# Kernel optimization log

Hardware: AMD Instinct MI355X
Metric: run time of the kernel (lower is better)

## Reference

```python
import jax, jax.numpy as jnp
import numpy as np

N_GENES = 20000
N_CELLS = 1024   # expression_dim
FM_DIM = 512     # scgpt_embed_dim
EMB = 512        # embed_dim == projection_dim
N_EDGES = 640000
EPS = 1e-5


def _layernorm(x, g, b):
    mu = jnp.mean(x, axis=-1, keepdims=True)
    var = jnp.mean((x - mu) ** 2, axis=-1, keepdims=True)
    return (x - mu) * jax.lax.rsqrt(var + EPS) * g + b


def _sage_conv(x, src, dst, Wl, bl, Wr):
    # PyG SAGEConv (mean aggr): lin_l(mean_{j in N(i)} x_j) + lin_r(x_i)
    n = x.shape[0]
    agg = jax.ops.segment_sum(x[src], dst, num_segments=n)          # [N, F]
    cnt = jax.ops.segment_sum(jnp.ones((src.shape[0],), x.dtype), dst, num_segments=n)
    mean = agg / jnp.maximum(cnt, 1.0)[:, None]
    return mean @ Wl.T + bl + x @ Wr.T


def setup_inputs() -> dict:
    key = jax.random.key(0)
    ks = jax.random.split(key, 20)
    s = 0.02
    inp = {
        'x_foundation': jax.random.normal(ks[0], (N_GENES, FM_DIM), jnp.float32),
        'x_expression': jax.random.normal(ks[1], (N_GENES, N_CELLS), jnp.float32),
        'ppi_edge_index': jax.random.randint(ks[2], (2, N_EDGES), 0, N_GENES, jnp.int32),
        # expression SAGE layer 0 (N_CELLS -> EMB)
        'Wl0': s * jax.random.normal(ks[3], (EMB, N_CELLS), jnp.float32),
        'bl0': jnp.zeros((EMB,), jnp.float32),
        'Wr0': s * jax.random.normal(ks[4], (EMB, N_CELLS), jnp.float32),
        # expression SAGE layer 1 (EMB -> EMB)
        'Wl1': s * jax.random.normal(ks[5], (EMB, EMB), jnp.float32),
        'bl1': jnp.zeros((EMB,), jnp.float32),
        'Wr1': s * jax.random.normal(ks[6], (EMB, EMB), jnp.float32),
        # foundation projection: Linear + LayerNorm
        'Wf': s * jax.random.normal(ks[7], (EMB, FM_DIM), jnp.float32),
        'bf': jnp.zeros((EMB,), jnp.float32),
        'g1': jnp.ones((EMB,), jnp.float32),
        'b1': jnp.zeros((EMB,), jnp.float32),
        # fusion layer: Linear + LayerNorm
        'Wfu': s * jax.random.normal(ks[8], (EMB, EMB), jnp.float32),
        'bfu': jnp.zeros((EMB,), jnp.float32),
        'g2': jnp.ones((EMB,), jnp.float32),
        'b2': jnp.zeros((EMB,), jnp.float32),
        # final SAGE layer (EMB -> EMB), max(1, num_layers//2) == 1 layer
        'Wl2': s * jax.random.normal(ks[9], (EMB, EMB), jnp.float32),
        'bl2': jnp.zeros((EMB,), jnp.float32),
        'Wr2': s * jax.random.normal(ks[10], (EMB, EMB), jnp.float32),
    }
    return inp


def reference(x_foundation, x_expression, ppi_edge_index,
              Wl0, bl0, Wr0, Wl1, bl1, Wr1,
              Wf, bf, g1, b1, Wfu, bfu, g2, b2,
              Wl2, bl2, Wr2):
    src, dst = ppi_edge_index[0], ppi_edge_index[1]
    # expression branch: SAGEConv -> ELU (dropout = identity in eval)
    h = jax.nn.elu(_sage_conv(x_expression, src, dst, Wl0, bl0, Wr0))
    h = jax.nn.elu(_sage_conv(h, src, dst, Wl1, bl1, Wr1))
    # foundation branch: Linear -> LayerNorm -> GELU (exact, as torch nn.GELU)
    f = jax.nn.gelu(_layernorm(x_foundation @ Wf.T + bf, g1, b1), approximate=False)
    # add fusion, then Linear -> LayerNorm -> SiLU
    fused = h + f
    fo = jax.nn.silu(_layernorm(fused @ Wfu.T + bfu, g2, b2))
    # final SAGE layer(s): SAGEConv -> ELU
    gene_emb = jax.nn.elu(_sage_conv(fo, src, dst, Wl2, bl2, Wr2))
    return gene_emb
```

## Files before the change

### kernel.cpp

```cpp
#include <hip/hip_runtime.h>
#include <hip/hip_bf16.h>
#include <math.h>

#define N_GENES 20000
#define N_CELLS 1024
#define FM_DIM  512
#define EMB     512
#define N_EDGES 640000
#define LN_EPS  1e-5f
#define SCAN_B  79
#define IDX_CAP 2560

typedef __attribute__((ext_vector_type(8))) short bf8;
typedef __attribute__((ext_vector_type(4))) float f32x4;

__device__ __forceinline__ float bflo(unsigned v) { return __uint_as_float(v << 16); }
__device__ __forceinline__ float bfhi(unsigned v) { return __uint_as_float(v & 0xffff0000u); }
__device__ __forceinline__ unsigned short f2bf(float f) {
    unsigned u = __float_as_uint(f);
    return (unsigned short)((u + 0x7fffu + ((u >> 16) & 1u)) >> 16);
}
__device__ __forceinline__ unsigned packbf(float x, float y) {
    return (unsigned)f2bf(x) | ((unsigned)f2bf(y) << 16);
}
__device__ __forceinline__ unsigned addbf2(unsigned x, unsigned y) {
    return packbf(bflo(x) + bflo(y), bfhi(x) + bfhi(y));
}
__device__ __forceinline__ uint4 pack8(float4 a, float4 b) {
    uint4 o;
    o.x = packbf(a.x, a.y);
    o.y = packbf(a.z, a.w);
    o.z = packbf(b.x, b.y);
    o.w = packbf(b.z, b.w);
    return o;
}

__device__ __forceinline__ void gload16(const unsigned short* g, unsigned short* l) {
    __builtin_amdgcn_global_load_lds(
        (const __attribute__((address_space(1))) unsigned int*)g,
        (__attribute__((address_space(3))) unsigned int*)l, 16, 0, 0);
}

__global__ __launch_bounds__(256) void k_cvtcnt(const float4* __restrict__ xe,
                                                const float4* s0, const float4* s1,
                                                const float4* s2, const float4* s3,
                                                const float4* s4, const float4* s5,
                                                const float4* s6, const float4* s7,
                                                uint4* __restrict__ Xe,
                                                uint4* __restrict__ Wb,
                                                const int* __restrict__ edst,
                                                int* __restrict__ cnt,
                                                unsigned char* __restrict__ eslot) {
    if (blockIdx.x < 2048) {
        for (int i = blockIdx.x * 256 + threadIdx.x; i < 2560000 + 327680;
             i += 2048 * 256) {
            if (i < 2560000) {
                Xe[i] = pack8(xe[2 * i], xe[2 * i + 1]);
            } else {
                int w = i - 2560000;
                const float4* src; int off;
                if (w < 65536)       { src = s0; off = w; }
                else if (w < 131072) { src = s1; off = w - 65536; }
                else if (w < 163840) { src = s2; off = w - 131072; }
                else if (w < 196608) { src = s3; off = w - 163840; }
                else if (w < 229376) { src = s4; off = w - 196608; }
                else if (w < 262144) { src = s5; off = w - 229376; }
                else if (w < 294912) { src = s6; off = w - 262144; }
                else                 { src = s7; off = w - 294912; }
                Wb[w] = pack8(src[2 * off], src[2 * off + 1]);
            }
        }
    } else {
        int e = (blockIdx.x - 2048) * 256 + threadIdx.x;
        if (e < N_EDGES) {
            int old = atomicAdd(&cnt[edst[e]], 1);
            eslot[e] = (unsigned char)old;
        }
    }
}

__global__ __launch_bounds__(256) void k_scan1(const int* __restrict__ cnt,
                                               int* __restrict__ row_ptr,
                                               int* __restrict__ bsum) {
    __shared__ int wsum[4];
    int b = blockIdx.x, t = threadIdx.x;
    int i = b * 256 + t;
    int v = (i < N_GENES) ? cnt[i] : 0;
    int lane = t & 63, wv = t >> 6;
    int x = v;
#pragma unroll
    for (int off = 1; off < 64; off <<= 1) {
        int y = __shfl_up(x, off);
        if (lane >= off) x += y;
    }
    if (lane == 63) wsum[wv] = x;
    __syncthreads();
    if (t == 0) {
        int s = 0;
        for (int w = 0; w < 4; ++w) { int tmp = wsum[w]; wsum[w] = s; s += tmp; }
    }
    __syncthreads();
    int excl = x - v + wsum[wv];
    if (i < N_GENES) row_ptr[i] = excl;
    if (t == 255) bsum[b] = excl + v;
}

__global__ void k_scan2(const int* __restrict__ bsum, int* __restrict__ boff) {
    __shared__ int wsum[2];
    int t = threadIdx.x;
    int v = (t < SCAN_B) ? bsum[t] : 0;
    int lane = t & 63, wv = t >> 6;
    int x = v;
#pragma unroll
    for (int off = 1; off < 64; off <<= 1) {
        int y = __shfl_up(x, off);
        if (lane >= off) x += y;
    }
    if (lane == 63) wsum[wv] = x;
    __syncthreads();
    int add = (wv == 1) ? wsum[0] : 0;
    int excl = x - v + add;
    if (t < SCAN_B) boff[t] = excl;
    if (t == SCAN_B) boff[SCAN_B] = excl;
}

__global__ __launch_bounds__(256) void k_scan3(int* __restrict__ row_ptr,
                                               const int* __restrict__ boff) {
    int i = blockIdx.x * 256 + threadIdx.x;
    if (i < N_GENES) row_ptr[i] += boff[i >> 8];
    if (blockIdx.x == 0 && threadIdx.x == 0) row_ptr[N_GENES] = boff[SCAN_B];
}

__global__ __launch_bounds__(256) void k_gemm_pf(const unsigned short* __restrict__ A,
                                                 const unsigned short* __restrict__ Wl,
                                                 const unsigned short* __restrict__ Wr,
                                                 unsigned short* __restrict__ C0,
                                                 unsigned short* __restrict__ C1,
                                                 int M, int K,
                                                 const int* __restrict__ e_src,
                                                 const int* __restrict__ e_dst,
                                                 const int* __restrict__ row_ptr,
                                                 const unsigned char* __restrict__ eslot,
                                                 int* __restrict__ csr) {
    __shared__ __attribute__((aligned(16))) unsigned short As[3][128][32];
    __shared__ __attribute__((aligned(16))) unsigned short Bs[3][128][32];
    if (blockIdx.y >= 160) {
        int e = ((blockIdx.y - 160) * 8 + blockIdx.x) * 256 + threadIdx.x;
        if (e < N_EDGES) {
            int d = e_dst[e];
            csr[row_ptr[d] + (int)eslot[e]] = e_src[e];
        }
        return;
    }
    int m0 = (blockIdx.x * 20 + (blockIdx.y >> 3)) * 128;
    if (m0 >= M) return;
    int sel = blockIdx.y & 7;
    const unsigned short* W = (sel < 4) ? Wl : Wr;
    unsigned short* Cp = (sel < 4) ? C0 : C1;
    int n0 = (sel & 3) * 128;
    int tid = threadIdx.x;
    int lane = tid & 63;
    int w = tid >> 6, wr = w >> 1, wc = w & 1;

    int srow = tid >> 2, sch = tid & 3;
    int rA0 = min(m0 + srow, M - 1);
    int rA1 = min(m0 + srow + 64, M - 1);
    const unsigned short* gA0 = A + (size_t)rA0 * K + sch * 8;
    const unsigned short* gA1 = A + (size_t)rA1 * K + sch * 8;
    const unsigned short* gB0 = W + (size_t)(n0 + srow) * K + sch * 8;
    const unsigned short* gB1 = W + (size_t)(n0 + srow + 64) * K + sch * 8;

    f32x4 acc[4][4];
#pragma unroll
    for (int i = 0; i < 4; ++i)
#pragma unroll
        for (int j = 0; j < 4; ++j) acc[i][j] = (f32x4){0.f, 0.f, 0.f, 0.f};

    auto stage = [&](int b, int k0) {
        unsigned short* Ab = &As[b][0][0];
        unsigned short* Bb = &Bs[b][0][0];
        gload16(gA0 + k0, Ab + tid * 8);
        gload16(gA1 + k0, Ab + 64 * 32 + tid * 8);
        gload16(gB0 + k0, Bb + tid * 8);
        gload16(gB1 + k0, Bb + 64 * 32 + tid * 8);
    };
    auto compute = [&](int b) {
        const unsigned short* Ab = &As[b][0][0];
        const unsigned short* Bb = &Bs[b][0][0];
        bf8 af[4], bff[4];
#pragma unroll
        for (int f = 0; f < 4; ++f) {
            af[f]  = *(const bf8*)(Ab + (wr * 64 + f * 16 + (lane & 15)) * 32 + (lane >> 4) * 8);
            bff[f] = *(const bf8*)(Bb + (wc * 64 + f * 16 + (lane & 15)) * 32 + (lane >> 4) * 8);
        }
#pragma unroll
        for (int i = 0; i < 4; ++i)
#pragma unroll
            for (int j = 0; j < 4; ++j)
                acc[i][j] = __builtin_amdgcn_mfma_f32_16x16x32_bf16(af[i], bff[j],
                                                                    acc[i][j], 0, 0, 0);
    };

#define PF_STEP(CB, SB, ST, VM)                                  \
    stage(SB, (ST) * 32);                                        \
    asm volatile("s_waitcnt vmcnt(" #VM ")" ::: "memory");       \
    __builtin_amdgcn_s_barrier();                                \
    __builtin_amdgcn_sched_barrier(0);                           \
    compute(CB);                                                 \
    asm volatile("s_waitcnt lgkmcnt(0)" ::: "memory");           \
    __builtin_amdgcn_s_barrier();                                \
    __builtin_amdgcn_sched_barrier(0);

    const int NT = K / 32;
    stage(0, 0);
    stage(1, 32);
    for (int t = 0; t + 4 < NT; t += 3) {
        PF_STEP(0, 2, t + 2, 8)
        PF_STEP(1, 0, t + 3, 8)
        PF_STEP(2, 1, t + 4, 8)
    }
    asm volatile("s_waitcnt vmcnt(4)" ::: "memory");
    __builtin_amdgcn_s_barrier();
    __builtin_amdgcn_sched_barrier(0);
    compute(0);
    asm volatile("s_waitcnt lgkmcnt(0)" ::: "memory");
    __builtin_amdgcn_s_barrier();
    __builtin_amdgcn_sched_barrier(0);
    asm volatile("s_waitcnt vmcnt(0)" ::: "memory");
    __builtin_amdgcn_s_barrier();
    __builtin_amdgcn_sched_barrier(0);
    compute(1);
#undef PF_STEP

#pragma unroll
    for (int i = 0; i < 4; ++i) {
        int rb = m0 + wr * 64 + i * 16 + (lane >> 4) * 4;
#pragma unroll
        for (int j = 0; j < 4; ++j) {
            int cc = n0 + wc * 64 + j * 16 + (lane & 15);
#pragma unroll
            for (int e = 0; e < 4; ++e) {
                int r = rb + e;
                if (r < M) Cp[(size_t)r * EMB + cc] = f2bf(acc[i][j][e]);
            }
        }
    }
}

__global__ __launch_bounds__(256) void k_gemm_fu(const unsigned short* __restrict__ A,
                                                 const unsigned short* __restrict__ A2,
                                                 const unsigned short* __restrict__ W,
                                                 unsigned short* __restrict__ Cp,
                                                 int M, int K) {
    __shared__ __attribute__((aligned(16))) unsigned short As[2][128][32];
    __shared__ __attribute__((aligned(16))) unsigned short Bs[2][128][32];
    int m0 = (blockIdx.x * 20 + (blockIdx.y >> 2)) * 128;
    if (m0 >= M) return;
    int n0 = (blockIdx.y & 3) * 128;
    int tid = threadIdx.x;
    int lane = tid & 63;
    int w = tid >> 6, wr = w >> 1, wc = w & 1;

    int srow = tid >> 2, sch = tid & 3;
    int rA0 = min(m0 + srow, M - 1);
    int rA1 = min(m0 + srow + 64, M - 1);
    const unsigned short* gA0 = A + (size_t)rA0 * K + sch * 8;
    const unsigned short* gA1 = A + (size_t)rA1 * K + sch * 8;
    const unsigned short* hA0 = A2 + (size_t)rA0 * K + sch * 8;
    const unsigned short* hA1 = A2 + (size_t)rA1 * K + sch * 8;
    const unsigned short* gB0 = W + (size_t)(n0 + srow) * K + sch * 8;
    const unsigned short* gB1 = W + (size_t)(n0 + srow + 64) * K + sch * 8;

    f32x4 acc[4][4];
#pragma unroll
    for (int i = 0; i < 4; ++i)
#pragma unroll
        for (int j = 0; j < 4; ++j) acc[i][j] = (f32x4){0.f, 0.f, 0.f, 0.f};

    auto compute = [&](int b) {
        const unsigned short* Ab = &As[b][0][0];
        const unsigned short* Bb = &Bs[b][0][0];
        bf8 af[4], bff[4];
#pragma unroll
        for (int f = 0; f < 4; ++f) {
            af[f]  = *(const bf8*)(Ab + (wr * 64 + f * 16 + (lane & 15)) * 32 + (lane >> 4) * 8);
            bff[f] = *(const bf8*)(Bb + (wc * 64 + f * 16 + (lane & 15)) * 32 + (lane >> 4) * 8);
        }
#pragma unroll
        for (int i = 0; i < 4; ++i)
#pragma unroll
            for (int j = 0; j < 4; ++j)
                acc[i][j] = __builtin_amdgcn_mfma_f32_16x16x32_bf16(af[i], bff[j],
                                                                    acc[i][j], 0, 0, 0);
    };

    for (int k0 = 0; k0 < K; k0 += 64) {
        uint4 x00 = *(const uint4*)(gA0 + k0);
        uint4 y00 = *(const uint4*)(hA0 + k0);
        uint4 x10 = *(const uint4*)(gA1 + k0);
        uint4 y10 = *(const uint4*)(hA1 + k0);
        uint4 x01 = *(const uint4*)(gA0 + k0 + 32);
        uint4 y01 = *(const uint4*)(hA0 + k0 + 32);
        uint4 x11 = *(const uint4*)(gA1 + k0 + 32);
        uint4 y11 = *(const uint4*)(hA1 + k0 + 32);
        uint4 a00, a10, a01, a11;
        a00.x = addbf2(x00.x, y00.x); a00.y = addbf2(x00.y, y00.y);
        a00.z = addbf2(x00.z, y00.z); a00.w = addbf2(x00.w, y00.w);
        a10.x = addbf2(x10.x, y10.x); a10.y = addbf2(x10.y, y10.y);
        a10.z = addbf2(x10.z, y10.z); a10.w = addbf2(x10.w, y10.w);
        a01.x = addbf2(x01.x, y01.x); a01.y = addbf2(x01.y, y01.y);
        a01.z = addbf2(x01.z, y01.z); a01.w = addbf2(x01.w, y01.w);
        a11.x = addbf2(x11.x, y11.x); a11.y = addbf2(x11.y, y11.y);
        a11.z = addbf2(x11.z, y11.z); a11.w = addbf2(x11.w, y11.w);
        __syncthreads();
        *(uint4*)(&As[0][0][0] + tid * 8)       = a00;
        *(uint4*)(&As[0][64][0] + tid * 8)      = a10;
        *(uint4*)(&As[1][0][0] + tid * 8)       = a01;
        *(uint4*)(&As[1][64][0] + tid * 8)      = a11;
        gload16(gB0 + k0,      &Bs[0][0][0] + tid * 8);
        gload16(gB1 + k0,      &Bs[0][64][0] + tid * 8);
        gload16(gB0 + k0 + 32, &Bs[1][0][0] + tid * 8);
        gload16(gB1 + k0 + 32, &Bs[1][64][0] + tid * 8);
        __syncthreads();
        compute(0);
        compute(1);
    }

#pragma unroll
    for (int i = 0; i < 4; ++i) {
        int rb = m0 + wr * 64 + i * 16 + (lane >> 4) * 4;
#pragma unroll
        for (int j = 0; j < 4; ++j) {
            int cc = n0 + wc * 64 + j * 16 + (lane & 15);
#pragma unroll
            for (int e = 0; e < 4; ++e) {
                int r = rb + e;
                if (r < M) Cp[(size_t)r * EMB + cc] = f2bf(acc[i][j][e]);
            }
        }
    }
}

__global__ __launch_bounds__(256) void k_gemm_p(const unsigned short* __restrict__ A,
                                                const unsigned short* __restrict__ Wl,
                                                const unsigned short* __restrict__ Wr,
                                                unsigned short* __restrict__ C0,
                                                unsigned short* __restrict__ C1,
                                                int M, int K) {
    __shared__ __attribute__((aligned(16))) unsigned short As[2][128][32];
    __shared__ __attribute__((aligned(16))) unsigned short Bs[2][128][32];
    int m0 = (blockIdx.x * 20 + (blockIdx.y >> 3)) * 128;
    if (m0 >= M) return;
    int sel = blockIdx.y & 7;
    const unsigned short* W = (sel < 4) ? Wl : Wr;
    unsigned short* Cp = (sel < 4) ? C0 : C1;
    int n0 = (sel & 3) * 128;
    int tid = threadIdx.x;
    int lane = tid & 63;
    int w = tid >> 6, wr = w >> 1, wc = w & 1;

    int srow = tid >> 2, sch = tid & 3;
    int rA0 = min(m0 + srow, M - 1);
    int rA1 = min(m0 + srow + 64, M - 1);
    const unsigned short* gA0 = A + (size_t)rA0 * K + sch * 8;
    const unsigned short* gA1 = A + (size_t)rA1 * K + sch * 8;
    const unsigned short* gB0 = W + (size_t)(n0 + srow) * K + sch * 8;
    const unsigned short* gB1 = W + (size_t)(n0 + srow + 64) * K + sch * 8;

    f32x4 acc[4][4];
#pragma unroll
    for (int i = 0; i < 4; ++i)
#pragma unroll
        for (int j = 0; j < 4; ++j) acc[i][j] = (f32x4){0.f, 0.f, 0.f, 0.f};

    auto compute = [&](int b) {
        const unsigned short* Ab = &As[b][0][0];
        const unsigned short* Bb = &Bs[b][0][0];
        bf8 af[4], bff[4];
#pragma unroll
        for (int f = 0; f < 4; ++f) {
            af[f]  = *(const bf8*)(Ab + (wr * 64 + f * 16 + (lane & 15)) * 32 + (lane >> 4) * 8);
            bff[f] = *(const bf8*)(Bb + (wc * 64 + f * 16 + (lane & 15)) * 32 + (lane >> 4) * 8);
        }
#pragma unroll
        for (int i = 0; i < 4; ++i)
#pragma unroll
            for (int j = 0; j < 4; ++j)
                acc[i][j] = __builtin_amdgcn_mfma_f32_16x16x32_bf16(af[i], bff[j],
                                                                    acc[i][j], 0, 0, 0);
    };

    for (int k0 = 0; k0 < K; k0 += 64) {
        __syncthreads();
        gload16(gA0 + k0,      &As[0][0][0] + tid * 8);
        gload16(gA1 + k0,      &As[0][64][0] + tid * 8);
        gload16(gA0 + k0 + 32, &As[1][0][0] + tid * 8);
        gload16(gA1 + k0 + 32, &As[1][64][0] + tid * 8);
        gload16(gB0 + k0,      &Bs[0][0][0] + tid * 8);
        gload16(gB1 + k0,      &Bs[0][64][0] + tid * 8);
        gload16(gB0 + k0 + 32, &Bs[1][0][0] + tid * 8);
        gload16(gB1 + k0 + 32, &Bs[1][64][0] + tid * 8);
        __syncthreads();
        compute(0);
        compute(1);
    }

#pragma unroll
    for (int i = 0; i < 4; ++i) {
        int rb = m0 + wr * 64 + i * 16 + (lane >> 4) * 4;
#pragma unroll
        for (int j = 0; j < 4; ++j) {
            int cc = n0 + wc * 64 + j * 16 + (lane & 15);
#pragma unroll
            for (int e = 0; e < 4; ++e) {
                int r = rb + e;
                if (r < M) Cp[(size_t)r * EMB + cc] = f2bf(acc[i][j][e]);
            }
        }
    }
}

__global__ __launch_bounds__(256) void k_gemm_3(const unsigned short* __restrict__ A1,
                                                const float* __restrict__ A2,
                                                const unsigned short* __restrict__ Wl,
                                                const unsigned short* __restrict__ Wr,
                                                const unsigned short* __restrict__ Wf,
                                                unsigned short* __restrict__ C0,
                                                unsigned short* __restrict__ C1,
                                                unsigned short* __restrict__ CF,
                                                int M) {
    const int K = 512;
    __shared__ __attribute__((aligned(16))) unsigned short As[2][128][32];
    __shared__ __attribute__((aligned(16))) unsigned short Bs[2][128][32];
    int y = blockIdx.y;
    bool fpath = (y >= 160);
    int m0, n0;
    const unsigned short* W;
    unsigned short* Cp;
    if (!fpath) {
        m0 = (blockIdx.x * 20 + (y >> 3)) * 128;
        int sel = y & 7;
        W = (sel < 4) ? Wl : Wr;
        Cp = (sel < 4) ? C0 : C1;
        n0 = (sel & 3) * 128;
    } else {
        int y2 = y - 160;
        m0 = (blockIdx.x * 20 + (y2 >> 2)) * 128;
        n0 = (y2 & 3) * 128;
        W = Wf;
        Cp = CF;
    }
    if (m0 >= M) return;
    int tid = threadIdx.x;
    int lane = tid & 63;
    int w = tid >> 6, wr = w >> 1, wc = w & 1;

    int srow = tid >> 2, sch = tid & 3;
    int rA0 = min(m0 + srow, M - 1);
    int rA1 = min(m0 + srow + 64, M - 1);
    const unsigned short* gA0 = A1 + (size_t)rA0 * K + sch * 8;
    const unsigned short* gA1 = A1 + (size_t)rA1 * K + sch * 8;
    const float* fA0 = A2 + (size_t)rA0 * K + sch * 8;
    const float* fA1 = A2 + (size_t)rA1 * K + sch * 8;
    const unsigned short* gB0 = W + (size_t)(n0 + srow) * K + sch * 8;
    const unsigned short* gB1 = W + (size_t)(n0 + srow + 64) * K + sch * 8;

    f32x4 acc[4][4];
#pragma unroll
    for (int i = 0; i < 4; ++i)
#pragma unroll
        for (int j = 0; j < 4; ++j) acc[i][j] = (f32x4){0.f, 0.f, 0.f, 0.f};

    auto compute = [&](int b) {
        const unsigned short* Ab = &As[b][0][0];
        const unsigned short* Bb = &Bs[b][0][0];
        bf8 af[4], bff[4];
#pragma unroll
        for (int f = 0; f < 4; ++f) {
            af[f]  = *(const bf8*)(Ab + (wr * 64 + f * 16 + (lane & 15)) * 32 + (lane >> 4) * 8);
            bff[f] = *(const bf8*)(Bb + (wc * 64 + f * 16 + (lane & 15)) * 32 + (lane >> 4) * 8);
        }
#pragma unroll
        for (int i = 0; i < 4; ++i)
#pragma unroll
            for (int j = 0; j < 4; ++j)
                acc[i][j] = __builtin_amdgcn_mfma_f32_16x16x32_bf16(af[i], bff[j],
                                                                    acc[i][j], 0, 0, 0);
    };

    for (int k0 = 0; k0 < K; k0 += 64) {
        float4 f0a, f0b, f0c, f0d, f1a, f1b, f1c, f1d;
        if (fpath) {
            f0a = *(const float4*)(fA0 + k0);      f0b = *(const float4*)(fA0 + k0 + 4);
            f1a = *(const float4*)(fA1 + k0);      f1b = *(const float4*)(fA1 + k0 + 4);
            f0c = *(const float4*)(fA0 + k0 + 32); f0d = *(const float4*)(fA0 + k0 + 36);
            f1c = *(const float4*)(fA1 + k0 + 32); f1d = *(const float4*)(fA1 + k0 + 36);
        }
        __syncthreads();
        if (fpath) {
            *(uint4*)(&As[0][0][0] + tid * 8)  = pack8(f0a, f0b);
            *(uint4*)(&As[0][64][0] + tid * 8) = pack8(f1a, f1b);
            *(uint4*)(&As[1][0][0] + tid * 8)  = pack8(f0c, f0d);
            *(uint4*)(&As[1][64][0] + tid * 8) = pack8(f1c, f1d);
        } else {
            gload16(gA0 + k0,      &As[0][0][0] + tid * 8);
            gload16(gA1 + k0,      &As[0][64][0] + tid * 8);
            gload16(gA0 + k0 + 32, &As[1][0][0] + tid * 8);
            gload16(gA1 + k0 + 32, &As[1][64][0] + tid * 8);
        }
        gload16(gB0 + k0,      &Bs[0][0][0] + tid * 8);
        gload16(gB1 + k0,      &Bs[0][64][0] + tid * 8);
        gload16(gB0 + k0 + 32, &Bs[1][0][0] + tid * 8);
        gload16(gB1 + k0 + 32, &Bs[1][64][0] + tid * 8);
        __syncthreads();
        compute(0);
        compute(1);
    }

#pragma unroll
    for (int i = 0; i < 4; ++i) {
        int rb = m0 + wr * 64 + i * 16 + (lane >> 4) * 4;
#pragma unroll
        for (int j = 0; j < 4; ++j) {
            int cc = n0 + wc * 64 + j * 16 + (lane & 15);
#pragma unroll
            for (int e = 0; e < 4; ++e) {
                int r = rb + e;
                if (r < M) Cp[(size_t)r * EMB + cc] = f2bf(acc[i][j][e]);
            }
        }
    }
}

template <int OUTF32>
__device__ __forceinline__ void sage_body(const unsigned short* yl,
                                          const unsigned short* yr,
                                          const float* bl,
                                          const int* row_ptr,
                                          const int* csr,
                                          void* outp, int slice, int nblk,
                                          int* sIdx) {
    int g = threadIdx.x >> 3;
    int l = threadIdx.x & 7;
    int node = nblk * 32 + g;
    int w = slice * 8 + l;
    int s32 = row_ptr[nblk * 32];
    int e32 = row_ptr[nblk * 32 + 32];
    int nIdx = e32 - s32;
    bool lds_ok = (nIdx <= IDX_CAP);
    if (lds_ok) {
        for (int i = threadIdx.x; i < nIdx; i += 256) sIdx[i] = csr[s32 + i];
    }
    __syncthreads();
    int s = row_ptr[node], e = row_ptr[node + 1];
    int deg = e - s;
    const char* Yb = (const char*)yl;
    unsigned lb = (unsigned)(w << 4);
    float ac[8];
#pragma unroll
    for (int q = 0; q < 8; ++q) ac[q] = 0.f;
    if (lds_ok) {
        int lp = s - s32;
        int p = 0;
        for (; p + 8 <= deg; p += 8) {
            int j[8];
#pragma unroll
            for (int q = 0; q < 8; ++q) j[q] = sIdx[lp + p + q];
            uint4 v[8];
#pragma unroll
            for (int q = 0; q < 8; ++q)
                v[q] = *(const uint4*)(Yb + (((unsigned)j[q] << 10) + lb));
#pragma unroll
            for (int q = 0; q < 8; ++q) {
                ac[0] += bflo(v[q].x); ac[1] += bfhi(v[q].x);
                ac[2] += bflo(v[q].y); ac[3] += bfhi(v[q].y);
                ac[4] += bflo(v[q].z); ac[5] += bfhi(v[q].z);
                ac[6] += bflo(v[q].w); ac[7] += bfhi(v[q].w);
            }
        }
        for (; p < deg; ++p) {
            int j = sIdx[lp + p];
            uint4 v = *(const uint4*)(Yb + (((unsigned)j << 10) + lb));
            ac[0] += bflo(v.x); ac[1] += bfhi(v.x);
            ac[2] += bflo(v.y); ac[3] += bfhi(v.y);
            ac[4] += bflo(v.z); ac[5] += bfhi(v.z);
            ac[6] += bflo(v.w); ac[7] += bfhi(v.w);
        }
    } else {
        for (int p = s; p < e; ++p) {
            int j = csr[p];
            uint4 v = *(const uint4*)(Yb + (((unsigned)j << 10) + lb));
            ac[0] += bflo(v.x); ac[1] += bfhi(v.x);
            ac[2] += bflo(v.y); ac[3] += bfhi(v.y);
            ac[4] += bflo(v.z); ac[5] += bfhi(v.z);
            ac[6] += bflo(v.w); ac[7] += bfhi(v.w);
        }
    }
    float inv = 1.f / fmaxf((float)deg, 1.f);
    uint4 vr = ((const uint4*)yr)[(size_t)node * 64 + w];
    float4 bA = ((const float4*)bl)[2 * w];
    float4 bB = ((const float4*)bl)[2 * w + 1];
    float o[8];
    o[0] = ac[0] * inv + bA.x + bflo(vr.x);
    o[1] = ac[1] * inv + bA.y + bfhi(vr.x);
    o[2] = ac[2] * inv + bA.z + bflo(vr.y);
    o[3] = ac[3] * inv + bA.w + bfhi(vr.y);
    o[4] = ac[4] * inv + bB.x + bflo(vr.z);
    o[5] = ac[5] * inv + bB.y + bfhi(vr.z);
    o[6] = ac[6] * inv + bB.z + bflo(vr.w);
    o[7] = ac[7] * inv + bB.w + bfhi(vr.w);
#pragma unroll
    for (int q = 0; q < 8; ++q) o[q] = o[q] > 0.f ? o[q] : expm1f(o[q]);
    if (OUTF32) {
        float4* O = (float4*)outp;
        O[(size_t)node * 128 + 2 * w]     = make_float4(o[0], o[1], o[2], o[3]);
        O[(size_t)node * 128 + 2 * w + 1] = make_float4(o[4], o[5], o[6], o[7]);
    } else {
        uint4 ov;
        ov.x = packbf(o[0], o[1]);
        ov.y = packbf(o[2], o[3]);
        ov.z = packbf(o[4], o[5]);
        ov.w = packbf(o[6], o[7]);
        ((uint4*)outp)[(size_t)node * 64 + w] = ov;
    }
}

template <int OUTF32>
__global__ __launch_bounds__(256) void k_sage_b(const unsigned short* __restrict__ yl,
                                                const unsigned short* __restrict__ yr,
                                                const float* __restrict__ bl,
                                                const int* __restrict__ row_ptr,
                                                const int* __restrict__ csr,
                                                void* __restrict__ outp) {
    __shared__ int sIdx[IDX_CAP];
    sage_body<OUTF32>(yl, yr, bl, row_ptr, csr, outp, blockIdx.x, blockIdx.y, sIdx);
}

template <int ACT>
__device__ __forceinline__ void ln_body(const unsigned short* X,
                                        const float* bias, const float* g,
                                        const float* b, unsigned short* Y, int row) {
    __shared__ float red[8];
    int t = threadIdx.x;
    unsigned v = *(const unsigned*)(X + (size_t)row * EMB + 2 * t);
    float x0 = bflo(v) + bias[2 * t];
    float x1 = bfhi(v) + bias[2 * t + 1];
    float s = x0 + x1;
    float q = x0 * x0 + x1 * x1;
#pragma unroll
    for (int off = 32; off > 0; off >>= 1) {
        s += __shfl_down(s, off);
        q += __shfl_down(q, off);
    }
    int wave = t >> 6, lane = t & 63;
    if (lane == 0) { red[wave * 2] = s; red[wave * 2 + 1] = q; }
    __syncthreads();
    if (t == 0) {
        float ts = 0.f, tq = 0.f;
        for (int w = 0; w < 4; w++) { ts += red[w * 2]; tq += red[w * 2 + 1]; }
        red[0] = ts; red[1] = tq;
    }
    __syncthreads();
    float mu   = red[0] * (1.0f / 512.0f);
    float var  = red[1] * (1.0f / 512.0f) - mu * mu;
    float rstd = rsqrtf(var + LN_EPS);
    float y0 = (x0 - mu) * rstd * g[2 * t]     + b[2 * t];
    float y1 = (x1 - mu) * rstd * g[2 * t + 1] + b[2 * t + 1];
    if (ACT == 0) {
        y0 = 0.5f * y0 * (1.0f + erff(y0 * 0.70710678118654752440f));
        y1 = 0.5f * y1 * (1.0f + erff(y1 * 0.70710678118654752440f));
    } else {
        y0 = y0 / (1.0f + expf(-y0));
        y1 = y1 / (1.0f + expf(-y1));
    }
    ((unsigned*)Y)[(size_t)row * (EMB / 2) + t] = packbf(y0, y1);
}

template <int ACT>
__global__ __launch_bounds__(256) void k_ln_b(const unsigned short* __restrict__ X,
                                              const float* __restrict__ bias,
                                              const float* __restrict__ g,
                                              const float* __restrict__ b,
                                              unsigned short* __restrict__ Y) {
    ln_body<ACT>(X, bias, g, b, Y, blockIdx.x);
}

__global__ __launch_bounds__(256) void k_sageln(const unsigned short* __restrict__ C0,
                                                const unsigned short* __restrict__ C1,
                                                const float* __restrict__ bl1,
                                                const int* __restrict__ row_ptr,
                                                const int* __restrict__ csr,
                                                unsigned short* __restrict__ Pd,
                                                const unsigned short* __restrict__ F0,
                                                const float* __restrict__ bf_,
                                                const float* __restrict__ g1,
                                                const float* __restrict__ b1,
                                                unsigned short* __restrict__ fout) {
    __shared__ int sIdx[IDX_CAP];
    if (blockIdx.y < 625) {
        sage_body<0>(C0, C1, bl1, row_ptr, csr, Pd, blockIdx.x, blockIdx.y, sIdx);
    } else {
        ln_body<0>(F0, bf_, g1, b1, fout, (blockIdx.y - 625) * 8 + blockIdx.x);
    }
}

extern "C" void kernel_launch(void* const* d_in, const int* in_sizes, int n_in,
                              void* d_out, int out_size, void* d_ws, size_t ws_size,
                              hipStream_t stream) {
    const float* x_found = (const float*)d_in[0];
    const float* x_exp   = (const float*)d_in[1];
    const int*   ppi     = (const int*)d_in[2];
    const float* Wl0 = (const float*)d_in[3];
    const float* bl0 = (const float*)d_in[4];
    const float* Wr0 = (const float*)d_in[5];
    const float* Wl1 = (const float*)d_in[6];
    const float* bl1 = (const float*)d_in[7];
    const float* Wr1 = (const float*)d_in[8];
    const float* Wf  = (const float*)d_in[9];
    const float* bf_ = (const float*)d_in[10];
    const float* g1  = (const float*)d_in[11];
    const float* b1  = (const float*)d_in[12];
    const float* Wfu = (const float*)d_in[13];
    const float* bfu = (const float*)d_in[14];
    const float* g2  = (const float*)d_in[15];
    const float* b2  = (const float*)d_in[16];
    const float* Wl2 = (const float*)d_in[17];
    const float* bl2 = (const float*)d_in[18];
    const float* Wr2 = (const float*)d_in[19];

    const int* e_src = ppi;
    const int* e_dst = ppi + N_EDGES;

    char* ws = (char*)d_ws;
    unsigned short* C0   = (unsigned short*)(ws);
    unsigned short* C1   = (unsigned short*)(ws + 20480000);
    unsigned short* actA = (unsigned short*)(ws + 40960000);
    int* cnt     = (int*)(ws + 61440000);
    int* row_ptr = (int*)(ws + 61520000);
    unsigned char* eslot = (unsigned char*)(ws + 61600064);
    int* csr     = (int*)(ws + 62240064);
    unsigned short* Wb = (unsigned short*)(ws + 64800064);
    unsigned short* Wl0b = Wb;
    unsigned short* Wr0b = Wb + 524288;
    unsigned short* Wl1b = Wb + 1048576;
    unsigned short* Wr1b = Wb + 1310720;
    unsigned short* Wfb  = Wb + 1572864;
    unsigned short* Wfub = Wb + 1835008;
    unsigned short* Wl2b = Wb + 2097152;
    unsigned short* Wr2b = Wb + 2359296;
    int* bsum = (int*)(ws + 70042944);
    int* boff = (int*)(ws + 70043264);

    unsigned short* Xe = (unsigned short*)d_out;
    unsigned short* Pd = (unsigned short*)d_out;
    unsigned short* F0 = (unsigned short*)d_out + 10240000;

    hipMemsetAsync(cnt, 0, N_GENES * sizeof(int), stream);
    k_cvtcnt<<<4548, 256, 0, stream>>>((const float4*)x_exp,
                                       (const float4*)Wl0, (const float4*)Wr0,
                                       (const float4*)Wl1, (const float4*)Wr1,
                                       (const float4*)Wf,  (const float4*)Wfu,
                                       (const float4*)Wl2, (const float4*)Wr2,
                                       (uint4*)Xe, (uint4*)Wb, e_dst, cnt, eslot);
    k_scan1<<<SCAN_B, 256, 0, stream>>>(cnt, row_ptr, bsum);
    k_scan2<<<1, 128, 0, stream>>>(bsum, boff);
    k_scan3<<<SCAN_B, 256, 0, stream>>>(row_ptr, boff);

    dim3 gg(8, 80);
    dim3 gp(8, 160);
    dim3 g3(8, 240);
    dim3 gpf(8, 473);
    dim3 gs(8, 625);
    dim3 gsl(8, 3125);

    k_gemm_pf<<<gpf, 256, 0, stream>>>(Xe, Wl0b, Wr0b, C0, C1, N_GENES, N_CELLS,
                                       e_src, e_dst, row_ptr, eslot, csr);
    k_sage_b<0><<<gs, 256, 0, stream>>>(C0, C1, bl0, row_ptr, csr, actA);

    k_gemm_3<<<g3, 256, 0, stream>>>(actA, x_found, Wl1b, Wr1b, Wfb,
                                     C0, C1, F0, N_GENES);
    k_sageln<<<gsl, 256, 0, stream>>>(C0, C1, bl1, row_ptr, csr,
                                      Pd, F0, bf_, g1, b1, actA);

    k_gemm_fu<<<gg, 256, 0, stream>>>(Pd, actA, Wfub, C0, N_GENES, EMB);
    k_ln_b<1><<<N_GENES, 256, 0, stream>>>(C0, bfu, g2, b2, actA);

    k_gemm_p<<<gp, 256, 0, stream>>>(actA, Wl2b, Wr2b, C0, C1, N_GENES, EMB);
    k_sage_b<1><<<gs, 256, 0, stream>>>(C0, C1, bl2, row_ptr, csr, (float*)d_out);
}
```

Baseline: 413.7 us.

## Move foundation projection GEMM into first SAGE aggregation launch

The foundation-branch GEMM (x_foundation @ Wf) is taken out of the combined layer-1 GEMM and placed as extra blocks in the layer-0 SAGE aggregation kernel, which now has a shared LDS buffer used by both roles. The layer-1 Wl/Wr GEMM goes back to the plain k_gemm_p kernel. The aim is to overlap the memory-bound gather with the independent compute-bound GEMM and to shorten the critical path. In exchange, the SAGE blocks now reserve a larger LDS allocation, which may lower their occupancy.

```diff
diff --git a/kernel.cpp b/kernel.cpp
--- a/kernel.cpp
+++ b/kernel.cpp
@@ -420,118 +420,6 @@
     }
 }
 
-__global__ __launch_bounds__(256) void k_gemm_3(const unsigned short* __restrict__ A1,
-                                                const float* __restrict__ A2,
-                                                const unsigned short* __restrict__ Wl,
-                                                const unsigned short* __restrict__ Wr,
-                                                const unsigned short* __restrict__ Wf,
-                                                unsigned short* __restrict__ C0,
-                                                unsigned short* __restrict__ C1,
-                                                unsigned short* __restrict__ CF,
-                                                int M) {
-    const int K = 512;
-    __shared__ __attribute__((aligned(16))) unsigned short As[2][128][32];
-    __shared__ __attribute__((aligned(16))) unsigned short Bs[2][128][32];
-    int y = blockIdx.y;
-    bool fpath = (y >= 160);
-    int m0, n0;
-    const unsigned short* W;
-    unsigned short* Cp;
-    if (!fpath) {
-        m0 = (blockIdx.x * 20 + (y >> 3)) * 128;
-        int sel = y & 7;
-        W = (sel < 4) ? Wl : Wr;
-        Cp = (sel < 4) ? C0 : C1;
-        n0 = (sel & 3) * 128;
-    } else {
-        int y2 = y - 160;
-        m0 = (blockIdx.x * 20 + (y2 >> 2)) * 128;
-        n0 = (y2 & 3) * 128;
-        W = Wf;
-        Cp = CF;
-    }
-    if (m0 >= M) return;
-    int tid = threadIdx.x;
-    int lane = tid & 63;
-    int w = tid >> 6, wr = w >> 1, wc = w & 1;
-
-    int srow = tid >> 2, sch = tid & 3;
-    int rA0 = min(m0 + srow, M - 1);
-    int rA1 = min(m0 + srow + 64, M - 1);
-    const unsigned short* gA0 = A1 + (size_t)rA0 * K + sch * 8;
-    const unsigned short* gA1 = A1 + (size_t)rA1 * K + sch * 8;
-    const float* fA0 = A2 + (size_t)rA0 * K + sch * 8;
-    const float* fA1 = A2 + (size_t)rA1 * K + sch * 8;
-    const unsigned short* gB0 = W + (size_t)(n0 + srow) * K + sch * 8;
-    const unsigned short* gB1 = W + (size_t)(n0 + srow + 64) * K + sch * 8;
-
-    f32x4 acc[4][4];
-#pragma unroll
-    for (int i = 0; i < 4; ++i)
-#pragma unroll
-        for (int j = 0; j < 4; ++j) acc[i][j] = (f32x4){0.f, 0.f, 0.f, 0.f};
-
-    auto compute = [&](int b) {
-        const unsigned short* Ab = &As[b][0][0];
-        const unsigned short* Bb = &Bs[b][0][0];
-        bf8 af[4], bff[4];
-#pragma unroll
-        for (int f = 0; f < 4; ++f) {
-            af[f]  = *(const bf8*)(Ab + (wr * 64 + f * 16 + (lane & 15)) * 32 + (lane >> 4) * 8);
-            bff[f] = *(const bf8*)(Bb + (wc * 64 + f * 16 + (lane & 15)) * 32 + (lane >> 4) * 8);
-        }
-#pragma unroll
-        for (int i = 0; i < 4; ++i)
-#pragma unroll
-            for (int j = 0; j < 4; ++j)
-                acc[i][j] = __builtin_amdgcn_mfma_f32_16x16x32_bf16(af[i], bff[j],
-                                                                    acc[i][j], 0, 0, 0);
-    };
-
-    for (int k0 = 0; k0 < K; k0 += 64) {
-        float4 f0a, f0b, f0c, f0d, f1a, f1b, f1c, f1d;
-        if (fpath) {
-            f0a = *(const float4*)(fA0 + k0);      f0b = *(const float4*)(fA0 + k0 + 4);
-            f1a = *(const float4*)(fA1 + k0);      f1b = *(const float4*)(fA1 + k0 + 4);
-            f0c = *(const float4*)(fA0 + k0 + 32); f0d = *(const float4*)(fA0 + k0 + 36);
-            f1c = *(const float4*)(fA1 + k0 + 32); f1d = *(const float4*)(fA1 + k0 + 36);
-        }
-        __syncthreads();
-        if (fpath) {
-            *(uint4*)(&As[0][0][0] + tid * 8)  = pack8(f0a, f0b);
-            *(uint4*)(&As[0][64][0] + tid * 8) = pack8(f1a, f1b);
-            *(uint4*)(&As[1][0][0] + tid * 8)  = pack8(f0c, f0d);
-            *(uint4*)(&As[1][64][0] + tid * 8) = pack8(f1c, f1d);
-        } else {
-            gload16(gA0 + k0,      &As[0][0][0] + tid * 8);
-            gload16(gA1 + k0,      &As[0][64][0] + tid * 8);
-            gload16(gA0 + k0 + 32, &As[1][0][0] + tid * 8);
-            gload16(gA1 + k0 + 32, &As[1][64][0] + tid * 8);
-        }
-        gload16(gB0 + k0,      &Bs[0][0][0] + tid * 8);
-        gload16(gB1 + k0,      &Bs[0][64][0] + tid * 8);
-        gload16(gB0 + k0 + 32, &Bs[1][0][0] + tid * 8);
-        gload16(gB1 + k0 + 32, &Bs[1][64][0] + tid * 8);
-        __syncthreads();
-        compute(0);
-        compute(1);
-    }
-
-#pragma unroll
-    for (int i = 0; i < 4; ++i) {
-        int rb = m0 + wr * 64 + i * 16 + (lane >> 4) * 4;
-#pragma unroll
-        for (int j = 0; j < 4; ++j) {
-            int cc = n0 + wc * 64 + j * 16 + (lane & 15);
-#pragma unroll
-            for (int e = 0; e < 4; ++e) {
-                int r = rb + e;
-                if (r < M) Cp[(size_t)r * EMB + cc] = f2bf(acc[i][j][e]);
-            }
-        }
-    }
-}
-
 template <int OUTF32>
 __device__ __forceinline__ void sage_body(const unsigned short* yl,
                                           const unsigned short* yr,
@@ -634,6 +522,96 @@
                                                 void* __restrict__ outp) {
     __shared__ int sIdx[IDX_CAP];
     sage_body<OUTF32>(yl, yr, bl, row_ptr, csr, outp, blockIdx.x, blockIdx.y, sIdx);
+}
+
+__global__ __launch_bounds__(256) void k_sagewf(const unsigned short* __restrict__ C0,
+                                                const unsigned short* __restrict__ C1,
+                                                const float* __restrict__ bl0,
+                                                const int* __restrict__ row_ptr,
+                                                const int* __restrict__ csr,
+                                                unsigned short* __restrict__ actA,
+                                                const float* __restrict__ A2,
+                                                const unsigned short* __restrict__ Wf,
+                                                unsigned short* __restrict__ CF,
+                                                int M) {
+    __shared__ __attribute__((aligned(16))) unsigned short smem[4][128][32];
+    if (blockIdx.y < 625) {
+        sage_body<0>(C0, C1, bl0, row_ptr, csr, actA, blockIdx.x, blockIdx.y,
+                     (int*)&smem[0][0][0]);
+        return;
+    }
+    const int K = 512;
+    int y2 = blockIdx.y - 625;
+    int m0 = (blockIdx.x * 20 + (y2 >> 2)) * 128;
+    if (m0 >= M) return;
+    int n0 = (y2 & 3) * 128;
+    int tid = threadIdx.x;
+    int lane = tid & 63;
+    int w = tid >> 6, wr = w >> 1, wc = w & 1;
+
+    int srow = tid >> 2, sch = tid & 3;
+    int rA0 = min(m0 + srow, M - 1);
+    int rA1 = min(m0 + srow + 64, M - 1);
+    const float* fA0 = A2 + (size_t)rA0 * K + sch * 8;
+    const float* fA1 = A2 + (size_t)rA1 * K + sch * 8;
+    const unsigned short* gB0 = Wf + (size_t)(n0 + srow) * K + sch * 8;
+    const unsigned short* gB1 = Wf + (size_t)(n0 + srow + 64) * K + sch * 8;
+
+    f32x4 acc[4][4];
+#pragma unroll
+    for (int i = 0; i < 4; ++i)
+#pragma unroll
+        for (int j = 0; j < 4; ++j) acc[i][j] = (f32x4){0.f, 0.f, 0.f, 0.f};
+
+    auto compute = [&](int b) {
+        const unsigned short* Ab = &smem[b][0][0];
+        const unsigned short* Bb = &smem[2 + b][0][0];
+        bf8 af[4], bff[4];
+#pragma unroll
+        for (int f = 0; f < 4; ++f) {
+            af[f]  = *(const bf8*)(Ab + (wr * 64 + f * 16 + (lane & 15)) * 32 + (lane >> 4) * 8);
+            bff[f] = *(const bf8*)(Bb + (wc * 64 + f * 16 + (lane & 15)) * 32 + (lane >> 4) * 8);
+        }
+#pragma unroll
+        for (int i = 0; i < 4; ++i)
+#pragma unroll
+            for (int j = 0; j < 4; ++j)
+                acc[i][j] = __builtin_amdgcn_mfma_f32_16x16x32_bf16(af[i], bff[j],
+                                                                    acc[i][j], 0, 0, 0);
+    };
+
+    for (int k0 = 0; k0 < K; k0 += 64) {
+        float4 f0a = *(const float4*)(fA0 + k0);      float4 f0b = *(const float4*)(fA0 + k0 + 4);
+        float4 f1a = *(const float4*)(fA1 + k0);      float4 f1b = *(const float4*)(fA1 + k0 + 4);
+        float4 f0c = *(const float4*)(fA0 + k0 + 32); float4 f0d = *(const float4*)(fA0 + k0 + 36);
+        float4 f1c = *(const float4*)(fA1 + k0 + 32); float4 f1d = *(const float4*)(fA1 + k0 + 36);
+        __syncthreads();
+        *(uint4*)(&smem[0][0][0] + tid * 8)  = pack8(f0a, f0b);
+        *(uint4*)(&smem[0][64][0] + tid * 8) = pack8(f1a, f1b);
+        *(uint4*)(&smem[1][0][0] + tid * 8)  = pack8(f0c, f0d);
+        *(uint4*)(&smem[1][64][0] + tid * 8) = pack8(f1c, f1d);
+        gload16(gB0 + k0,      &smem[2][0][0] + tid * 8);
+        gload16(gB1 + k0,      &smem[2][64][0] + tid * 8);
+        gload16(gB0 + k0 + 32, &smem[3][0][0] + tid * 8);
+        gload16(gB1 + k0 + 32, &smem[3][64][0] + tid * 8);
+        __syncthreads();
+        compute(0);
+        compute(1);
+    }
+
+#pragma unroll
+    for (int i = 0; i < 4; ++i) {
+        int rb = m0 + wr * 64 + i * 16 + (lane >> 4) * 4;
+#pragma unroll
+        for (int j = 0; j < 4; ++j) {
+            int cc = n0 + wc * 64 + j * 16 + (lane & 15);
+#pragma unroll
+            for (int e = 0; e < 4; ++e) {
+                int r = rb + e;
+                if (r < M) CF[(size_t)r * EMB + cc] = f2bf(acc[i][j][e]);
+            }
+        }
+    }
 }
 
 template <int ACT>
@@ -768,17 +746,17 @@
 
     dim3 gg(8, 80);
     dim3 gp(8, 160);
-    dim3 g3(8, 240);
     dim3 gpf(8, 473);
     dim3 gs(8, 625);
+    dim3 gsw(8, 705);
     dim3 gsl(8, 3125);
 
     k_gemm_pf<<<gpf, 256, 0, stream>>>(Xe, Wl0b, Wr0b, C0, C1, N_GENES, N_CELLS,
                                        e_src, e_dst, row_ptr, eslot, csr);
-    k_sage_b<0><<<gs, 256, 0, stream>>>(C0, C1, bl0, row_ptr, csr, actA);
-
-    k_gemm_3<<<g3, 256, 0, stream>>>(actA, x_found, Wl1b, Wr1b, Wfb,
-                                     C0, C1, F0, N_GENES);
+    k_sagewf<<<gsw, 256, 0, stream>>>(C0, C1, bl0, row_ptr, csr, actA,
+                                      x_found, Wfb, F0, N_GENES);
+
+    k_gemm_p<<<gp, 256, 0, stream>>>(actA, Wl1b, Wr1b, C0, C1, N_GENES, EMB);
     k_sageln<<<gsl, 256, 0, stream>>>(C0, C1, bl1, row_ptr, csr,
                                       Pd, F0, bf_, g1, b1, actA);
 
```

New measurement: 448.6 us. 1.08x slower.
